# Optimization experiments

Hardware: AMD Instinct MI355X
Metric: run time of the kernel (lower is better)

Reference implementation:

```python
import jax, jax.numpy as jnp
import numpy as np
from functools import partial

N = 50000      # nodes
E = 800000     # edges
B = 64         # graphs in batch
D = 64         # embedding_dim (= per-head out_dim)
H = 2          # num_heads
G = 50         # n_gaussians
HID = 128      # hidden_dim of edge-filter net
MLP_DIM = 128  # mlp_dim of OutputMLP
OUT = 1        # output_dim
L = 3          # n_interactions
CUTOFF = 8.0
MEAN = 0.0
STD = 1.0


def ssp(x):
    # shifted softplus: softplus(x) - log(2)
    return jax.nn.softplus(x) - jnp.log(2.0)


def setup_inputs() -> dict:
    key = jax.random.key(0)
    ks = jax.random.split(key, 24)
    R = jax.random.normal(ks[0], (N, 3), dtype=jnp.float32) * 3.0
    Z = jax.random.randint(ks[1], (N,), 0, 100)
    src = jax.random.randint(ks[2], (E,), 0, N)
    dst = jax.random.randint(ks[3], (E,), 0, N)
    graph_ids = jnp.sort(jax.random.randint(ks[4], (N,), 0, B))
    # embedding table with padding_idx=0 zeroed
    emb_table = (jax.random.normal(ks[5], (100, D), dtype=jnp.float32) * 0.1).at[0].set(0.0)
    offsets = jnp.linspace(0.0, CUTOFF, G, dtype=jnp.float32)
    widths = jnp.full((G,), offsets[1] - offsets[0], dtype=jnp.float32)
    s = 0.1
    rn = lambda k, shp: jax.random.normal(k, shp, dtype=jnp.float32) * s
    return {
        "R": R, "Z": Z, "src": src, "dst": dst, "graph_ids": graph_ids,
        "emb_table": emb_table, "offsets": offsets, "widths": widths,
        "fc_w": rn(ks[6], (L, D, H * D)),
        "attn_l": rn(ks[7], (L, H, D)),
        "attn_r": rn(ks[8], (L, H, D)),
        "filt_w1": rn(ks[9], (L, G, HID)), "filt_b1": jnp.zeros((L, HID), jnp.float32),
        "filt_w2": rn(ks[10], (L, HID, H * D)), "filt_b2": jnp.zeros((L, H * D), jnp.float32),
        "mlp_w1": rn(ks[11], (L, H * D, D)), "mlp_b1": jnp.zeros((L, D), jnp.float32),
        "mlp_w2": rn(ks[12], (L, D, D)), "mlp_b2": jnp.zeros((L, D), jnp.float32),
        "out_w1": rn(ks[13], (D, MLP_DIM)), "out_b1": jnp.zeros((MLP_DIM,), jnp.float32),
        "out_w2": rn(ks[14], (MLP_DIM, OUT)), "out_b2": jnp.zeros((OUT,), jnp.float32),
    }


def _forward(R, emb_table, offsets, widths, fc_w, attn_l, attn_r,
             filt_w1, filt_b1, filt_w2, filt_b2,
             mlp_w1, mlp_b1, mlp_w2, mlp_b2,
             out_w1, out_b1, out_w2, out_b2,
             Z, src, dst, graph_ids):
    # per-edge distances
    r = jnp.linalg.norm(R[src] - R[dst], axis=1)  # (E,)
    # Gaussian smearing (trainable offsets/widths, schnetpack style)
    coeff = -0.5 / (widths ** 2)
    gs = jnp.exp(coeff * (r[:, None] - offsets) ** 2)  # (E, G)
    # cosine cutoff
    C = 0.5 * (jnp.cos(r * (jnp.pi / CUTOFF)) + 1.0) * (r < CUTOFF).astype(r.dtype)  # (E,)
    x = emb_table[Z]  # (N, D)
    for l in range(L):
        h = (x @ fc_w[l]).reshape(N, H, D)  # (N, H, D)
        # cfconv-style edge filter from gaussian features
        w = ssp(gs @ filt_w1[l] + filt_b1[l]) @ filt_w2[l] + filt_b2[l]  # (E, H*D)
        w = w.reshape(E, H, D)
        msg = h[src] * w * C[:, None, None]  # (E, H, D)
        # GAT attention, softmax over incoming edges per dst node
        el = jnp.einsum('nhd,hd->nh', h, attn_l[l])
        er = jnp.einsum('nhd,hd->nh', h, attn_r[l])
        e = jax.nn.leaky_relu(el[src] + er[dst], negative_slope=0.2)  # (E, H)
        m = jax.ops.segment_max(e, dst, num_segments=N)  # (N, H)
        ex = jnp.exp(e - m[dst])
        denom = jax.ops.segment_sum(ex, dst, num_segments=N)  # (N, H)
        alpha = ex / denom[dst]  # (E, H)
        agg = jax.ops.segment_sum(alpha[:, :, None] * msg, dst, num_segments=N)  # (N, H, D)
        v = ssp(agg).reshape(N, H * D)
        v = ssp(v @ mlp_w1[l] + mlp_b1[l]) @ mlp_w2[l] + mlp_b2[l]  # (N, D)
        x = x + v
    hh = ssp(x @ out_w1 + out_b1) @ out_w2 + out_b2  # (N, OUT)
    hh = hh * STD + MEAN
    return jax.ops.segment_sum(hh, graph_ids, num_segments=B)  # (B, OUT)


def reference(R, Z, src, dst, graph_ids, emb_table, offsets, widths,
              fc_w, attn_l, attn_r, filt_w1, filt_b1, filt_w2, filt_b2,
              mlp_w1, mlp_b1, mlp_w2, mlp_b2,
              out_w1, out_b1, out_w2, out_b2):
    return _forward(R, emb_table, offsets, widths, fc_w, attn_l, attn_r,
                    filt_w1, filt_b1, filt_w2, filt_b2,
                    mlp_w1, mlp_b1, mlp_w2, mlp_b2,
                    out_w1, out_b1, out_w2, out_b2,
                    Z, src, dst, graph_ids)
```

## Files before the change

kernel.cpp:

```cpp
#include <hip/hip_runtime.h>
#include <stdint.h>

#define N_NODES 50000
#define N_EDGES 800000
#define B_GRAPHS 64
#define D_DIM 64
#define HD 128
#define G_GAUSS 50
#define HID_DIM 128
#define L_LAYERS 3
#define LN2 0.69314718055994530942f
#define PI_OVER_8 0.39269908169872414f
#define NCHUNK 196

#define TN 64
#define TLD 132
#define XLD 68
#define NBLK ((N_NODES + TN - 1) / TN)

#define LUT_T 2048
#define LUT_INV_STEP 256.0f
#define LROWS 8

__device__ __forceinline__ float sspf(float x) {
    float ax = fabsf(x);
    return fmaxf(x, 0.f) + __logf(1.f + __expf(-ax)) - LN2;
}
__device__ __forceinline__ unsigned short f2bf(float f) {
    union { float f; unsigned int i; } v; v.f = f;
    unsigned int u = v.i;
    return (unsigned short)((u + 0x7FFFu + ((u >> 16) & 1u)) >> 16);
}

__global__ void repr_prep(int* __restrict__ count_f, int* __restrict__ count_s,
                          float* __restrict__ dout) {
    int i = blockIdx.x * 256 + threadIdx.x;
    if (i < N_NODES) count_f[i] = 0;
    else if (i < 2 * N_NODES) count_s[i - N_NODES] = 0;
    else if (i < 2 * N_NODES + B_GRAPHS) dout[i - 2 * N_NODES] = 0.f;
}

__global__ __launch_bounds__(256) void repr_lut_build(
    const float* __restrict__ offs, const float* __restrict__ widths,
    const float* __restrict__ fw1, const float* __restrict__ fb1,
    const float* __restrict__ fw2, const float* __restrict__ fb2,
    unsigned int* __restrict__ lut)
{
    __shared__ float gs_s[LROWS + 1][G_GAUSS];
    __shared__ float hid_s[LROWS + 1][HID_DIM];
    __shared__ float wc_s[LROWS + 1][HD];
    const int nb = LUT_T / LROWS;
    int l = blockIdx.x / nb;
    int i0r = (blockIdx.x % nb) * LROWS;
    int tid = threadIdx.x;
    const float step = 8.0f / LUT_T;

    for (int j = tid; j < (LROWS + 1) * G_GAUSS; j += 256) {
        int r = j / G_GAUSS, k = j - r * G_GAUSS;
        float rr = (i0r + r) * step;
        float wdt = widths[k];
        float dr = rr - offs[k];
        gs_s[r][k] = expf(-0.5f / (wdt * wdt) * dr * dr);
    }
    __syncthreads();

    int c = tid & 127, sub = tid >> 7;
    int rlo = sub * 4;
    {
        const float* W1 = fw1 + (size_t)l * G_GAUSS * HID_DIM + c;
        float acc[5];
        float bb = fb1[l * HID_DIM + c];
        #pragma unroll
        for (int r = 0; r < 5; r++) acc[r] = bb;
        for (int k = 0; k < G_GAUSS; k++) {
            float wv = W1[k * HID_DIM];
            #pragma unroll
            for (int r = 0; r < 5; r++)
                acc[r] = fmaf(gs_s[rlo + r][k], wv, acc[r]);
        }
        #pragma unroll
        for (int r = 0; r < 5; r++) hid_s[rlo + r][c] = sspf(acc[r]);
    }
    __syncthreads();
    {
        const float* W2 = fw2 + (size_t)l * HID_DIM * HD + c;
        float acc[5];
        float bb = fb2[l * HD + c];
        #pragma unroll
        for (int r = 0; r < 5; r++) acc[r] = bb;
        for (int k = 0; k < HID_DIM; k++) {
            float wv = W2[k * HD];
            #pragma unroll
            for (int r = 0; r < 5; r++)
                acc[r] = fmaf(hid_s[rlo + r][k], wv, acc[r]);
        }
        #pragma unroll
        for (int r = 0; r < 5; r++) {
            float rr = (i0r + rlo + r) * step;
            float C = (rr < 8.0f) ? 0.5f * (cosf(rr * PI_OVER_8) + 1.f) : 0.f;
            wc_s[rlo + r][c] = acc[r] * C;
        }
    }
    __syncthreads();
    for (int j = tid; j < LROWS * HD; j += 256) {
        int r = j >> 7, cc = j & 127;
        unsigned int lo = f2bf(wc_s[r][cc]);
        unsigned int hi = f2bf(wc_s[r + 1][cc]);
        lut[((size_t)l * LUT_T + i0r + r) * HD + cc] = lo | (hi << 16);
    }
}

__global__ void repr_hist(const float* __restrict__ R,
                          const int* __restrict__ src, const int* __restrict__ dst,
                          int* __restrict__ count_f, int* __restrict__ count_s,
                          float* __restrict__ r_full) {
    int e = blockIdx.x * blockDim.x + threadIdx.x;
    if (e >= N_EDGES) return;
    int s = src[e], d = dst[e];
    atomicAdd(&count_f[d], 1);
    float dx = R[3*s+0] - R[3*d+0];
    float dy = R[3*s+1] - R[3*d+1];
    float dz = R[3*s+2] - R[3*d+2];
    float r = sqrtf(dx*dx + dy*dy + dz*dz);
    r_full[e] = r;
    if (r < 8.0f) atomicAdd(&count_s[d], 1);
}

__global__ void repr_scanA2(const int* __restrict__ cntA, int* __restrict__ exclA,
                            int* __restrict__ bsumA,
                            const int* __restrict__ cntB, int* __restrict__ exclB,
                            int* __restrict__ bsumB) {
    __shared__ int tmp[256];
    int t = threadIdx.x, b = blockIdx.x;
    const int* cnt; int* excl; int* bsum; int bb;
    if (b < NCHUNK) { cnt = cntA; excl = exclA; bsum = bsumA; bb = b; }
    else            { cnt = cntB; excl = exclB; bsum = bsumB; bb = b - NCHUNK; }
    int i = bb * 256 + t;
    int v = (i < N_NODES) ? cnt[i] : 0;
    tmp[t] = v; __syncthreads();
    for (int off = 1; off < 256; off <<= 1) {
        int add = (t >= off) ? tmp[t - off] : 0;
        __syncthreads();
        tmp[t] += add;
        __syncthreads();
    }
    if (i < N_NODES) excl[i] = tmp[t] - v;
    if (t == 255) bsum[bb] = tmp[255];
}
__global__ void repr_scanB2(const int* __restrict__ bsumA, int* __restrict__ bprefA,
                            int* __restrict__ ecA,
                            const int* __restrict__ bsumB, int* __restrict__ bprefB,
                            int* __restrict__ ecB) {
    __shared__ int tmp[256];
    const int* bsum = blockIdx.x ? bsumB : bsumA;
    int* bpref = blockIdx.x ? bprefB : bprefA;
    int* ec = blockIdx.x ? ecB : ecA;
    int t = threadIdx.x;
    int v = (t < NCHUNK) ? bsum[t] : 0;
    tmp[t] = v; __syncthreads();
    for (int off = 1; off < 256; off <<= 1) {
        int add = (t >= off) ? tmp[t - off] : 0;
        __syncthreads();
        tmp[t] += add;
        __syncthreads();
    }
    if (t < NCHUNK) bpref[t] = tmp[t] - v;
    if (t == 255) ec[0] = tmp[255];
}
__global__ void repr_scanC2(const int* __restrict__ exclA, const int* __restrict__ bprefA,
                            int* __restrict__ curA, int* __restrict__ rowptr,
                            const int* __restrict__ exclB, const int* __restrict__ bprefB,
                            int* __restrict__ curB) {
    int b = blockIdx.x;
    if (b < NCHUNK) {
        int i = b * 256 + threadIdx.x;
        if (i < N_NODES) { int v = exclA[i] + bprefA[b]; curA[i] = v; rowptr[i] = v; }
    } else {
        int i = (b - NCHUNK) * 256 + threadIdx.x;
        if (i < N_NODES) curB[i] = exclB[i] + bprefB[b - NCHUNK];
    }
}

__global__ void repr_scatter(const float* __restrict__ r_full,
                             const int* __restrict__ src, const int* __restrict__ dst,
                             int* __restrict__ cur_f, int* __restrict__ cur_s,
                             unsigned short* __restrict__ ssrc_f,
                             int2* __restrict__ surv) {
    int e = blockIdx.x * blockDim.x + threadIdx.x;
    if (e >= N_EDGES) return;
    int s = src[e], d = dst[e];
    float r = r_full[e];
    int pos = atomicAdd(&cur_f[d], 1);
    ssrc_f[pos] = (unsigned short)s;
    if (r < 8.0f) {
        int p2 = atomicAdd(&cur_s[d], 1);
        unsigned rf = (unsigned)fminf(r * 16777216.f, 134217727.f);
        surv[p2] = make_int2((int)((unsigned)s | ((unsigned)d << 16)), (int)rf);
    }
}


__device__ __forceinline__ void load_ssp_agg(int base, int tid,
        const float* __restrict__ agg, float* __restrict__ bufA) {
    int row = tid >> 2;
    int c0 = (tid & 3) << 5;
    const float* ap = agg + (size_t)(base + row) * HD + c0;
    float* tp = bufA + row * TLD + c0;
    #pragma unroll
    for (int j = 0; j < 8; j++) {
        float4 v = *(const float4*)(ap + j * 4);
        tp[j*4+0] = sspf(v.x); tp[j*4+1] = sspf(v.y);
        tp[j*4+2] = sspf(v.z); tp[j*4+3] = sspf(v.w);
    }
}

__device__ __forceinline__ void gemm_mlp(int base, int tid,
        const float* __restrict__ w1, const float* __restrict__ b1,
        const float* __restrict__ w2, const float* __restrict__ b2,
        float* __restrict__ x, float* __restrict__ bufA, float* __restrict__ v1s)
{
    const int rg = tid >> 4, cg = tid & 15;
    const int r0 = rg * 4, c0 = cg * 4;
    float acc[4][4];
    #pragma unroll
    for (int r = 0; r < 4; r++)
        #pragma unroll
        for (int c = 0; c < 4; c++) acc[r][c] = 0.f;
    for (int k0 = 0; k0 < 128; k0 += 4) {
        float av[4][4];
        #pragma unroll
        for (int r = 0; r < 4; r++)
            *(float4*)av[r] = *(const float4*)&bufA[(r0 + r) * TLD + k0];
        #pragma unroll
        for (int kk = 0; kk < 4; kk++) {
            float4 wv = *(const float4*)(w1 + (k0 + kk) * 64 + c0);
            float wf[4] = {wv.x, wv.y, wv.z, wv.w};
            #pragma unroll
            for (int r = 0; r < 4; r++)
                #pragma unroll
                for (int c = 0; c < 4; c++)
                    acc[r][c] = fmaf(av[r][kk], wf[c], acc[r][c]);
        }
    }
    {
        float4 bv = *(const float4*)(b1 + c0);
        float ba[4] = {bv.x, bv.y, bv.z, bv.w};
        #pragma unroll
        for (int r = 0; r < 4; r++)
            #pragma unroll
            for (int c = 0; c < 4; c++)
                v1s[(r0 + r) * XLD + c0 + c] = sspf(acc[r][c] + ba[c]);
    }
    __syncthreads();
    float acc2[4][4];
    #pragma unroll
    for (int r = 0; r < 4; r++)
        #pragma unroll
        for (int c = 0; c < 4; c++) acc2[r][c] = 0.f;
    for (int k0 = 0; k0 < 64; k0 += 4) {
        float av[4][4];
        #pragma unroll
        for (int r = 0; r < 4; r++)
            *(float4*)av[r] = *(const float4*)&v1s[(r0 + r) * XLD + k0];
        #pragma unroll
        for (int kk = 0; kk < 4; kk++) {
            float4 wv = *(const float4*)(w2 + (k0 + kk) * 64 + c0);
            float wf[4] = {wv.x, wv.y, wv.z, wv.w};
            #pragma unroll
            for (int r = 0; r < 4; r++)
                #pragma unroll
                for (int c = 0; c < 4; c++)
                    acc2[r][c] = fmaf(av[r][kk], wf[c], acc2[r][c]);
        }
    }
    {
        float4 bv = *(const float4*)(b2 + c0);
        #pragma unroll
        for (int r = 0; r < 4; r++) {
            int n = base + r0 + r;
            float4 xv = *(const float4*)(x + (size_t)n * 64 + c0);
            float4 o;
            o.x = acc2[r][0] + bv.x + xv.x;
            o.y = acc2[r][1] + bv.y + xv.y;
            o.z = acc2[r][2] + bv.z + xv.z;
            o.w = acc2[r][3] + bv.w + xv.w;
            *(float4*)&bufA[(r0 + r) * XLD + c0] = o;
            if (n < N_NODES) *(float4*)(x + (size_t)n * 64 + c0) = o;
        }
    }
    __syncthreads();
}

__device__ __forceinline__ void gemm_h(int base, int tid,
        const float* __restrict__ bufA,
        const float* __restrict__ fc_w, const float* __restrict__ attn_l,
        const float* __restrict__ attn_r,
        unsigned int* __restrict__ hq, float* __restrict__ el, float* __restrict__ er)
{
    const int rg = tid >> 4, cg = tid & 15;
    const int r0 = rg * 4, c0 = cg * 8;
    float acc[4][8];
    #pragma unroll
    for (int r = 0; r < 4; r++)
        #pragma unroll
        for (int c = 0; c < 8; c++) acc[r][c] = 0.f;
    for (int k0 = 0; k0 < 64; k0 += 4) {
        float av[4][4];
        #pragma unroll
        for (int r = 0; r < 4; r++)
            *(float4*)av[r] = *(const float4*)&bufA[(r0 + r) * XLD + k0];
        #pragma unroll
        for (int kk = 0; kk < 4; kk++) {
            float4 w0 = *(const float4*)(fc_w + (k0 + kk) * 128 + c0);
            float4 w1v = *(const float4*)(fc_w + (k0 + kk) * 128 + c0 + 4);
            float wf[8] = {w0.x, w0.y, w0.z, w0.w, w1v.x, w1v.y, w1v.z, w1v.w};
            #pragma unroll
            for (int r = 0; r < 4; r++)
                #pragma unroll
                for (int c = 0; c < 8; c++)
                    acc[r][c] = fmaf(av[r][kk], wf[c], acc[r][c]);
        }
    }
    float al[8], ar[8];
    #pragma unroll
    for (int c = 0; c < 8; c++) { al[c] = attn_l[c0 + c]; ar[c] = attn_r[c0 + c]; }
    int head = cg >> 3;
    #pragma unroll
    for (int r = 0; r < 4; r++) {
        int n = base + r0 + r;
        float pel = 0.f, per = 0.f;
        #pragma unroll
        for (int c = 0; c < 8; c++) {
            pel = fmaf(acc[r][c], al[c], pel);
            per = fmaf(acc[r][c], ar[c], per);
        }
        if (n < N_NODES) {
            uint4 pv;
            pv.x = (unsigned int)f2bf(acc[r][0]) | ((unsigned int)f2bf(acc[r][1]) << 16);
            pv.y = (unsigned int)f2bf(acc[r][2]) | ((unsigned int)f2bf(acc[r][3]) << 16);
            pv.z = (unsigned int)f2bf(acc[r][4]) | ((unsigned int)f2bf(acc[r][5]) << 16);
            pv.w = (unsigned int)f2bf(acc[r][6]) | ((unsigned int)f2bf(acc[r][7]) << 16);
            *(uint4*)(hq + (size_t)n * 64 + cg * 4) = pv;
        }
        #pragma unroll
        for (int off = 1; off < 8; off <<= 1) {
            pel += __shfl_xor(pel, off, 64);
            per += __shfl_xor(per, off, 64);
        }
        if ((cg & 7) == 0 && n < N_NODES) {
            el[n * 2 + head] = pel;
            er[n * 2 + head] = per;
        }
    }
}

__global__ __launch_bounds__(256) void repr_embed_h(
        const float* __restrict__ emb, const int* __restrict__ Z,
        const float* __restrict__ fc_w, const float* __restrict__ attn_l,
        const float* __restrict__ attn_r,
        float* __restrict__ x, unsigned int* __restrict__ hq,
        float* __restrict__ el, float* __restrict__ er) {
    __shared__ float bufA[TN * XLD];
    int base = blockIdx.x * TN, tid = threadIdx.x;
    int row = tid >> 2;
    int c0 = (tid & 3) << 4;
    int n = base + row;
    int z = (n < N_NODES) ? Z[n] : 0;
    const float* ep = emb + (size_t)z * D_DIM + c0;
    float* bp = bufA + row * XLD + c0;
    #pragma unroll
    for (int j = 0; j < 4; j++) {
        float4 v = *(const float4*)(ep + j * 4);
        *(float4*)(bp + j * 4) = v;
        if (n < N_NODES) *(float4*)(x + (size_t)n * D_DIM + c0 + j * 4) = v;
    }
    __syncthreads();
    gemm_h(base, tid, bufA, fc_w, attn_l, attn_r, hq, el, er);
}

__global__ __launch_bounds__(256) void repr_mlp_h(
        const float* __restrict__ agg,
        const float* __restrict__ w1, const float* __restrict__ b1,
        const float* __restrict__ w2, const float* __restrict__ b2,
        const float* __restrict__ fc_w, const float* __restrict__ attn_l,
        const float* __restrict__ attn_r,
        float* __restrict__ x, unsigned int* __restrict__ hq,
        float* __restrict__ el, float* __restrict__ er) {
    __shared__ float bufA[TN * TLD];
    __shared__ float v1s[TN * XLD];
    int base = blockIdx.x * TN, tid = threadIdx.x;
    load_ssp_agg(base, tid, agg, bufA);
    __syncthreads();
    gemm_mlp(base, tid, w1, b1, w2, b2, x, bufA, v1s);
    gemm_h(base, tid, bufA, fc_w, attn_l, attn_r, hq, el, er);
}

__global__ __launch_bounds__(256) void repr_mlp_out(
        const float* __restrict__ agg,
        const float* __restrict__ w1, const float* __restrict__ b1,
        const float* __restrict__ w2, const float* __restrict__ b2,
        const float* __restrict__ ow1, const float* __restrict__ ob1,
        const float* __restrict__ ow2, const float* __restrict__ ob2,
        float* __restrict__ x, float* __restrict__ hh) {
    __shared__ float bufA[TN * TLD];
    __shared__ float v1s[TN * XLD];
    int base = blockIdx.x * TN, tid = threadIdx.x;
    load_ssp_agg(base, tid, agg, bufA);
    __syncthreads();
    gemm_mlp(base, tid, w1, b1, w2, b2, x, bufA, v1s);
    const int rg = tid >> 4, cg = tid & 15;
    const int r0 = rg * 4, c0 = cg * 8;
    float acc[4][8];
    #pragma unroll
    for (int r = 0; r < 4; r++)
        #pragma unroll
        for (int c = 0; c < 8; c++) acc[r][c] = 0.f;
    for (int k0 = 0; k0 < 64; k0 += 4) {
        float av[4][4];
        #pragma unroll
        for (int r = 0; r < 4; r++)
            *(float4*)av[r] = *(const float4*)&bufA[(r0 + r) * XLD + k0];
        #pragma unroll
        for (int kk = 0; kk < 4; kk++) {
            float4 w0 = *(const float4*)(ow1 + (k0 + kk) * 128 + c0);
            float4 w1v = *(const float4*)(ow1 + (k0 + kk) * 128 + c0 + 4);
            float wf[8] = {w0.x, w0.y, w0.z, w0.w, w1v.x, w1v.y, w1v.z, w1v.w};
            #pragma unroll
            for (int r = 0; r < 4; r++)
                #pragma unroll
                for (int c = 0; c < 8; c++)
                    acc[r][c] = fmaf(av[r][kk], wf[c], acc[r][c]);
        }
    }
    float o1[8], w2c[8];
    #pragma unroll
    for (int c = 0; c < 8; c++) { o1[c] = ob1[c0 + c]; w2c[c] = ow2[c0 + c]; }
    #pragma unroll
    for (int r = 0; r < 4; r++) {
        int n = base + r0 + r;
        float s = 0.f;
        #pragma unroll
        for (int c = 0; c < 8; c++)
            s = fmaf(sspf(acc[r][c] + o1[c]), w2c[c], s);
        #pragma unroll
        for (int off = 1; off < 16; off <<= 1)
            s += __shfl_xor(s, off, 64);
        if (cg == 0 && n < N_NODES) hh[n] = s + ob2[0];
    }
}

__global__ void repr_alpha(const unsigned short* __restrict__ ssrc_f,
                           const int* __restrict__ rowptr,
                           const float* __restrict__ el, const float* __restrict__ er,
                           float2* __restrict__ md, float* __restrict__ agg) {
    int t = blockIdx.x * 256 + threadIdx.x;
    int d = t >> 4;
    int lane16 = t & 15;
    if (d >= N_NODES) return;
    float4 z = make_float4(0.f, 0.f, 0.f, 0.f);
    float4* ar = (float4*)(agg + (size_t)d * HD);
    ar[lane16 * 2] = z;
    ar[lane16 * 2 + 1] = z;
    int rs = rowptr[d];
    int re = (d == N_NODES - 1) ? N_EDGES : rowptr[d + 1];
    float2 erd = *(const float2*)&er[2 * d];
    float s0 = 0.f, s1 = 0.f;
    for (int i = rs + lane16; i < re; i += 16) {
        int s = ssrc_f[i];
        float2 a = *(const float2*)&el[2 * s];
        float v0 = a.x + erd.x; v0 = v0 >= 0.f ? v0 : 0.2f * v0;
        float v1 = a.y + erd.y; v1 = v1 >= 0.f ? v1 : 0.2f * v1;
        s0 += __expf(v0);
        s1 += __expf(v1);
    }
    #pragma unroll
    for (int off = 8; off > 0; off >>= 1) {
        s0 += __shfl_xor(s0, off, 64);
        s1 += __shfl_xor(s1, off, 64);
    }
    if (lane16 == 0) md[d] = make_float2(1.f / s0, 1.f / s1);
}

#define TILE 64
__global__ __launch_bounds__(256) void repr_msg_lut(
    const int2* __restrict__ surv, const int* __restrict__ ecount,
    const float* __restrict__ el, const float* __restrict__ er,
    const float2* __restrict__ md, const unsigned int* __restrict__ hq,
    const unsigned int* __restrict__ lut,
    float* __restrict__ agg)
{
    __shared__ int4 rowinfo[TILE];
    __shared__ float scl[TILE][2];
    int EC = ecount[0];
    int base = blockIdx.x * TILE;
    if (base >= EC) return;
    int tid = threadIdx.x;
    if (tid < TILE) {
        int i = base + tid;
        int sn = 0, d = -1, i0 = 0;
        float fr = 0.f, sc0 = 0.f, sc1 = 0.f;
        if (i < EC) {
            int2 ev = surv[i];
            sn = (int)((unsigned)ev.x & 0xFFFFu);
            d  = (int)((unsigned)ev.x >> 16);
            unsigned rf = (unsigned)ev.y;
            i0 = (int)(rf >> 16);
            fr = (float)(rf & 0xFFFFu) * (1.f / 65536.f);
            float2 a = *(const float2*)&el[2 * sn];
            float2 b = *(const float2*)&er[2 * d];
            float2 rd = md[d];
            float v0 = a.x + b.x; v0 = v0 >= 0.f ? v0 : 0.2f * v0;
            float v1 = a.y + b.y; v1 = v1 >= 0.f ? v1 : 0.2f * v1;
            sc0 = __expf(v0) * rd.x;
            sc1 = __expf(v1) * rd.y;
        }
        rowinfo[tid] = make_int4(i0, sn, d, __float_as_int(fr));
        scl[tid][0] = sc0; scl[tid][1] = sc1;
    }
    __syncthreads();
    const int cp = tid & 63;
    const int sp = tid >> 6;
    const int head = cp >> 5;
    const int lo = sp * 16;
    const uint2* __restrict__ l2p = (const uint2*)lut;
    float sum0 = 0.f, sum1 = 0.f;
    int cur_d = -1;
    int seg_first = 1;
    #pragma unroll 4
    for (int j = 0; j < 16; j++) {
        int r = lo + j;
        int4 ri = rowinfo[r];
        if (ri.z != cur_d) {
            if (cur_d >= 0) {
                float* ap = &agg[(size_t)cur_d * HD + 2 * cp];
                if (seg_first) { atomicAdd(ap, sum0); atomicAdd(ap + 1, sum1); }
                else *(float2*)ap = make_float2(sum0, sum1);
            }
            cur_d = ri.z; sum0 = 0.f; sum1 = 0.f; seg_first = (j == 0);
        }
        if (ri.z >= 0) {
            uint2 tv = l2p[(size_t)ri.x * 64 + cp];
            float fr = __int_as_float(ri.w);
            float wa0 = __uint_as_float(tv.x << 16);
            float wa1 = __uint_as_float(tv.x & 0xFFFF0000u);
            float wb0 = __uint_as_float(tv.y << 16);
            float wb1 = __uint_as_float(tv.y & 0xFFFF0000u);
            unsigned int hv = hq[(size_t)ri.y * 64 + cp];
            float ha = __uint_as_float(hv << 16);
            float hb = __uint_as_float(hv & 0xFFFF0000u);
            float s = scl[r][head];
            float wa = fmaf(fr, wa1 - wa0, wa0);
            float wb = fmaf(fr, wb1 - wb0, wb0);
            sum0 = fmaf(wa * ha, s, sum0);
            sum1 = fmaf(wb * hb, s, sum1);
        }
    }
    if (cur_d >= 0) {
        float* ap = &agg[(size_t)cur_d * HD + 2 * cp];
        atomicAdd(ap, sum0); atomicAdd(ap + 1, sum1);
    }
}

__global__ void repr_gsum(const float* __restrict__ hh, const int* __restrict__ gids,
                          float* __restrict__ dout) {
    __shared__ float bins[B_GRAPHS];
    int t = threadIdx.x;
    if (t < B_GRAPHS) bins[t] = 0.f;
    __syncthreads();
    int i = blockIdx.x * 256 + t;
    if (i < N_NODES) atomicAdd(&bins[gids[i]], hh[i]);
    __syncthreads();
    if (t < B_GRAPHS && bins[t] != 0.f) atomicAdd(&dout[t], bins[t]);
}

extern "C" void kernel_launch(void* const* d_in, const int* in_sizes, int n_in,
                              void* d_out, int out_size, void* d_ws, size_t ws_size,
                              hipStream_t stream) {
    (void)in_sizes; (void)n_in; (void)out_size; (void)ws_size;
    const float* R      = (const float*)d_in[0];
    const int*   Z      = (const int*)d_in[1];
    const int*   src    = (const int*)d_in[2];
    const int*   dst    = (const int*)d_in[3];
    const int*   gids   = (const int*)d_in[4];
    const float* emb    = (const float*)d_in[5];
    const float* offs   = (const float*)d_in[6];
    const float* widths = (const float*)d_in[7];
    const float* fc_w   = (const float*)d_in[8];
    const float* attn_l = (const float*)d_in[9];
    const float* attn_r = (const float*)d_in[10];
    const float* fw1    = (const float*)d_in[11];
    const float* fb1    = (const float*)d_in[12];
    const float* fw2    = (const float*)d_in[13];
    const float* fb2    = (const float*)d_in[14];
    const float* mw1    = (const float*)d_in[15];
    const float* mb1    = (const float*)d_in[16];
    const float* mw2    = (const float*)d_in[17];
    const float* mb2    = (const float*)d_in[18];
    const float* ow1    = (const float*)d_in[19];
    const float* ob1    = (const float*)d_in[20];
    const float* ow2    = (const float*)d_in[21];
    const float* ob2    = (const float*)d_in[22];

    char* p = (char*)d_ws;
    float* x      = (float*)p; p += (size_t)N_NODES * 64 * 4;
    unsigned int* hq = (unsigned int*)p; p += (size_t)N_NODES * 64 * 4;
    float* el     = (float*)p; p += (size_t)N_NODES * 2 * 4;
    float* er     = (float*)p; p += (size_t)N_NODES * 2 * 4;
    float2* md    = (float2*)p; p += (size_t)N_NODES * 8;
    float* agg    = (float*)p; p += (size_t)N_NODES * 128 * 4;
    unsigned short* ssrc_f = (unsigned short*)p; p += (size_t)N_EDGES * 2;
    int*   rowptr = (int*)p;   p += (size_t)N_NODES * 4;
    int2*  surv   = (int2*)p;  p += (size_t)N_EDGES * 8;
    float* r_full = (float*)p; p += (size_t)N_EDGES * 4;
    float* hh     = (float*)p; p += (size_t)N_NODES * 4;
    int*   bsumA  = (int*)p;   p += 1024;
    int*   bprefA = (int*)p;   p += 1024;
    int*   bsumB  = (int*)p;   p += 1024;
    int*   bprefB = (int*)p;   p += 1024;
    int*   ecF    = (int*)p;   p += 256;
    int*   ecS    = (int*)p;   p += 256;
    unsigned int* lut = (unsigned int*)r_full;
    int* count_f = (int*)x;
    int* excl_f  = (int*)((char*)x + 256 * 1024);
    int* cur_f   = (int*)((char*)x + 512 * 1024);
    int* count_s = (int*)((char*)x + 768 * 1024);
    int* excl_s  = (int*)((char*)x + 1024 * 1024);
    int* cur_s   = (int*)((char*)x + 1280 * 1024);

    repr_prep<<<(2 * N_NODES + B_GRAPHS + 255) / 256, 256, 0, stream>>>(
        count_f, count_s, (float*)d_out);
    repr_hist<<<N_EDGES / 256, 256, 0, stream>>>(R, src, dst, count_f, count_s, r_full);
    repr_scanA2<<<2 * NCHUNK, 256, 0, stream>>>(count_f, excl_f, bsumA,
                                                count_s, excl_s, bsumB);
    repr_scanB2<<<2, 256, 0, stream>>>(bsumA, bprefA, ecF, bsumB, bprefB, ecS);
    repr_scanC2<<<2 * NCHUNK, 256, 0, stream>>>(excl_f, bprefA, cur_f, rowptr,
                                                excl_s, bprefB, cur_s);
    repr_scatter<<<N_EDGES / 256, 256, 0, stream>>>(
        r_full, src, dst, cur_f, cur_s, ssrc_f, surv);

    repr_lut_build<<<L_LAYERS * (LUT_T / LROWS), 256, 0, stream>>>(
        offs, widths, fw1, fb1, fw2, fb2, lut);

    repr_embed_h<<<NBLK, 256, 0, stream>>>(
        emb, Z, fc_w, attn_l, attn_r, x, hq, el, er);

    for (int l = 0; l < L_LAYERS; l++) {
        repr_alpha<<<(N_NODES * 16 + 255) / 256, 256, 0, stream>>>(
            ssrc_f, rowptr, el, er, md, agg);
        repr_msg_lut<<<N_EDGES / TILE, 256, 0, stream>>>(
            surv, ecS, el, er, md, hq,
            lut + (size_t)l * LUT_T * HD, agg);
        if (l < L_LAYERS - 1) {
            repr_mlp_h<<<NBLK, 256, 0, stream>>>(
                agg, mw1 + (size_t)l * 128 * 64, mb1 + l * 64,
                mw2 + (size_t)l * 64 * 64, mb2 + l * 64,
                fc_w + (size_t)(l + 1) * 64 * 128, attn_l + (l + 1) * 128,
                attn_r + (l + 1) * 128, x, hq, el, er);
        } else {
            repr_mlp_out<<<NBLK, 256, 0, stream>>>(
                agg, mw1 + (size_t)l * 128 * 64, mb1 + l * 64,
                mw2 + (size_t)l * 64 * 64, mb2 + l * 64,
                ow1, ob1, ow2, ob2, x, hh);
        }
    }
    repr_gsum<<<NCHUNK, 256, 0, stream>>>(hh, gids, (float*)d_out);
}
```

Measured before the change: 692.0 us.

## Replace full-graph CSR softmax denominator with per-edge atomic accumulation

Drops the full-edge CSR build (count, scan and scatter for all edges) and its dst-sorted source array. Each layer now computes the softmax denominator with a per-edge kernel that atomically adds exp values into a per-node buffer. A second small kernel inverts the sums, resets the buffer and zeroes agg. This removes the setup cost of the second CSR pass but adds float atomics on 800k edges per layer, with random el gathers. The summation order also becomes nondeterministic.

```diff
diff --git a/kernel.cpp b/kernel.cpp
--- a/kernel.cpp
+++ b/kernel.cpp
@@ -19,7 +19,6 @@
 #define NBLK ((N_NODES + TN - 1) / TN)
 
 #define LUT_T 2048
-#define LUT_INV_STEP 256.0f
 #define LROWS 8
 
 __device__ __forceinline__ float sspf(float x) {
@@ -32,12 +31,12 @@
     return (unsigned short)((u + 0x7FFFu + ((u >> 16) & 1u)) >> 16);
 }
 
-__global__ void repr_prep(int* __restrict__ count_f, int* __restrict__ count_s,
+__global__ void repr_prep(int* __restrict__ count_s, float* __restrict__ denom,
                           float* __restrict__ dout) {
     int i = blockIdx.x * 256 + threadIdx.x;
-    if (i < N_NODES) count_f[i] = 0;
-    else if (i < 2 * N_NODES) count_s[i - N_NODES] = 0;
-    else if (i < 2 * N_NODES + B_GRAPHS) dout[i - 2 * N_NODES] = 0.f;
+    if (i < N_NODES) count_s[i] = 0;
+    else if (i < 3 * N_NODES) denom[i - N_NODES] = 0.f;
+    else if (i < 3 * N_NODES + B_GRAPHS) dout[i - 3 * N_NODES] = 0.f;
 }
 
 __global__ __launch_bounds__(256) void repr_lut_build(
@@ -112,12 +111,11 @@
 
 __global__ void repr_hist(const float* __restrict__ R,
                           const int* __restrict__ src, const int* __restrict__ dst,
-                          int* __restrict__ count_f, int* __restrict__ count_s,
+                          int* __restrict__ count_s,
                           float* __restrict__ r_full) {
     int e = blockIdx.x * blockDim.x + threadIdx.x;
     if (e >= N_EDGES) return;
     int s = src[e], d = dst[e];
-    atomicAdd(&count_f[d], 1);
     float dx = R[3*s+0] - R[3*d+0];
     float dy = R[3*s+1] - R[3*d+1];
     float dz = R[3*s+2] - R[3*d+2];
@@ -126,16 +124,11 @@
     if (r < 8.0f) atomicAdd(&count_s[d], 1);
 }
 
-__global__ void repr_scanA2(const int* __restrict__ cntA, int* __restrict__ exclA,
-                            int* __restrict__ bsumA,
-                            const int* __restrict__ cntB, int* __restrict__ exclB,
-                            int* __restrict__ bsumB) {
+__global__ void repr_scanA(const int* __restrict__ cnt, int* __restrict__ excl,
+                           int* __restrict__ bsum) {
     __shared__ int tmp[256];
     int t = threadIdx.x, b = blockIdx.x;
-    const int* cnt; int* excl; int* bsum; int bb;
-    if (b < NCHUNK) { cnt = cntA; excl = exclA; bsum = bsumA; bb = b; }
-    else            { cnt = cntB; excl = exclB; bsum = bsumB; bb = b - NCHUNK; }
-    int i = bb * 256 + t;
+    int i = b * 256 + t;
     int v = (i < N_NODES) ? cnt[i] : 0;
     tmp[t] = v; __syncthreads();
     for (int off = 1; off < 256; off <<= 1) {
@@ -145,16 +138,11 @@
         __syncthreads();
     }
     if (i < N_NODES) excl[i] = tmp[t] - v;
-    if (t == 255) bsum[bb] = tmp[255];
-}
-__global__ void repr_scanB2(const int* __restrict__ bsumA, int* __restrict__ bprefA,
-                            int* __restrict__ ecA,
-                            const int* __restrict__ bsumB, int* __restrict__ bprefB,
-                            int* __restrict__ ecB) {
+    if (t == 255) bsum[b] = tmp[255];
+}
+__global__ void repr_scanB(const int* __restrict__ bsum, int* __restrict__ bpref,
+                           int* __restrict__ ec) {
     __shared__ int tmp[256];
-    const int* bsum = blockIdx.x ? bsumB : bsumA;
-    int* bpref = blockIdx.x ? bprefB : bprefA;
-    int* ec = blockIdx.x ? ecB : ecA;
     int t = threadIdx.x;
     int v = (t < NCHUNK) ? bsum[t] : 0;
     tmp[t] = v; __syncthreads();
@@ -167,32 +155,21 @@
     if (t < NCHUNK) bpref[t] = tmp[t] - v;
     if (t == 255) ec[0] = tmp[255];
 }
-__global__ void repr_scanC2(const int* __restrict__ exclA, const int* __restrict__ bprefA,
-                            int* __restrict__ curA, int* __restrict__ rowptr,
-                            const int* __restrict__ exclB, const int* __restrict__ bprefB,
-                            int* __restrict__ curB) {
-    int b = blockIdx.x;
-    if (b < NCHUNK) {
-        int i = b * 256 + threadIdx.x;
-        if (i < N_NODES) { int v = exclA[i] + bprefA[b]; curA[i] = v; rowptr[i] = v; }
-    } else {
-        int i = (b - NCHUNK) * 256 + threadIdx.x;
-        if (i < N_NODES) curB[i] = exclB[i] + bprefB[b - NCHUNK];
-    }
+__global__ void repr_scanC(const int* __restrict__ excl, const int* __restrict__ bpref,
+                           int* __restrict__ cur) {
+    int i = blockIdx.x * 256 + threadIdx.x;
+    if (i < N_NODES) cur[i] = excl[i] + bpref[blockIdx.x];
 }
 
 __global__ void repr_scatter(const float* __restrict__ r_full,
                              const int* __restrict__ src, const int* __restrict__ dst,
-                             int* __restrict__ cur_f, int* __restrict__ cur_s,
-                             unsigned short* __restrict__ ssrc_f,
+                             int* __restrict__ cur_s,
                              int2* __restrict__ surv) {
     int e = blockIdx.x * blockDim.x + threadIdx.x;
     if (e >= N_EDGES) return;
-    int s = src[e], d = dst[e];
     float r = r_full[e];
-    int pos = atomicAdd(&cur_f[d], 1);
-    ssrc_f[pos] = (unsigned short)s;
     if (r < 8.0f) {
+        int s = src[e], d = dst[e];
         int p2 = atomicAdd(&cur_s[d], 1);
         unsigned rf = (unsigned)fminf(r * 16777216.f, 134217727.f);
         surv[p2] = make_int2((int)((unsigned)s | ((unsigned)d << 16)), (int)rf);
@@ -449,10 +426,22 @@
     }
 }
 
-__global__ void repr_alpha(const unsigned short* __restrict__ ssrc_f,
-                           const int* __restrict__ rowptr,
-                           const float* __restrict__ el, const float* __restrict__ er,
-                           float2* __restrict__ md, float* __restrict__ agg) {
+__global__ void repr_alpha_e(const int* __restrict__ src, const int* __restrict__ dst,
+                             const float* __restrict__ el, const float* __restrict__ er,
+                             float* __restrict__ denom) {
+    int e = blockIdx.x * 256 + threadIdx.x;
+    if (e >= N_EDGES) return;
+    int s = src[e], d = dst[e];
+    float2 a = *(const float2*)&el[2 * s];
+    float2 b = *(const float2*)&er[2 * d];
+    float v0 = a.x + b.x; v0 = v0 >= 0.f ? v0 : 0.2f * v0;
+    float v1 = a.y + b.y; v1 = v1 >= 0.f ? v1 : 0.2f * v1;
+    atomicAdd(&denom[2 * d],     __expf(v0));
+    atomicAdd(&denom[2 * d + 1], __expf(v1));
+}
+
+__global__ void repr_mdk(float* __restrict__ denom, float2* __restrict__ md,
+                         float* __restrict__ agg) {
     int t = blockIdx.x * 256 + threadIdx.x;
     int d = t >> 4;
     int lane16 = t & 15;
@@ -461,24 +450,11 @@
     float4* ar = (float4*)(agg + (size_t)d * HD);
     ar[lane16 * 2] = z;
     ar[lane16 * 2 + 1] = z;
-    int rs = rowptr[d];
-    int re = (d == N_NODES - 1) ? N_EDGES : rowptr[d + 1];
-    float2 erd = *(const float2*)&er[2 * d];
-    float s0 = 0.f, s1 = 0.f;
-    for (int i = rs + lane16; i < re; i += 16) {
-        int s = ssrc_f[i];
-        float2 a = *(const float2*)&el[2 * s];
-        float v0 = a.x + erd.x; v0 = v0 >= 0.f ? v0 : 0.2f * v0;
-        float v1 = a.y + erd.y; v1 = v1 >= 0.f ? v1 : 0.2f * v1;
-        s0 += __expf(v0);
-        s1 += __expf(v1);
-    }
-    #pragma unroll
-    for (int off = 8; off > 0; off >>= 1) {
-        s0 += __shfl_xor(s0, off, 64);
-        s1 += __shfl_xor(s1, off, 64);
-    }
-    if (lane16 == 0) md[d] = make_float2(1.f / s0, 1.f / s1);
+    if (lane16 == 0) {
+        float2 dn = *(const float2*)&denom[2 * d];
+        md[d] = make_float2(1.f / dn.x, 1.f / dn.y);
+        *(float2*)&denom[2 * d] = make_float2(0.f, 0.f);
+    }
 }
 
 #define TILE 64
@@ -607,36 +583,27 @@
     float* el     = (float*)p; p += (size_t)N_NODES * 2 * 4;
     float* er     = (float*)p; p += (size_t)N_NODES * 2 * 4;
     float2* md    = (float2*)p; p += (size_t)N_NODES * 8;
+    float* denom  = (float*)p; p += (size_t)N_NODES * 2 * 4;
     float* agg    = (float*)p; p += (size_t)N_NODES * 128 * 4;
-    unsigned short* ssrc_f = (unsigned short*)p; p += (size_t)N_EDGES * 2;
-    int*   rowptr = (int*)p;   p += (size_t)N_NODES * 4;
     int2*  surv   = (int2*)p;  p += (size_t)N_EDGES * 8;
     float* r_full = (float*)p; p += (size_t)N_EDGES * 4;
     float* hh     = (float*)p; p += (size_t)N_NODES * 4;
-    int*   bsumA  = (int*)p;   p += 1024;
-    int*   bprefA = (int*)p;   p += 1024;
-    int*   bsumB  = (int*)p;   p += 1024;
-    int*   bprefB = (int*)p;   p += 1024;
-    int*   ecF    = (int*)p;   p += 256;
+    int*   bsum   = (int*)p;   p += 1024;
+    int*   bpref  = (int*)p;   p += 1024;
     int*   ecS    = (int*)p;   p += 256;
     unsigned int* lut = (unsigned int*)r_full;
-    int* count_f = (int*)x;
-    int* excl_f  = (int*)((char*)x + 256 * 1024);
-    int* cur_f   = (int*)((char*)x + 512 * 1024);
-    int* count_s = (int*)((char*)x + 768 * 1024);
-    int* excl_s  = (int*)((char*)x + 1024 * 1024);
-    int* cur_s   = (int*)((char*)x + 1280 * 1024);
-
-    repr_prep<<<(2 * N_NODES + B_GRAPHS + 255) / 256, 256, 0, stream>>>(
-        count_f, count_s, (float*)d_out);
-    repr_hist<<<N_EDGES / 256, 256, 0, stream>>>(R, src, dst, count_f, count_s, r_full);
-    repr_scanA2<<<2 * NCHUNK, 256, 0, stream>>>(count_f, excl_f, bsumA,
-                                                count_s, excl_s, bsumB);
-    repr_scanB2<<<2, 256, 0, stream>>>(bsumA, bprefA, ecF, bsumB, bprefB, ecS);
-    repr_scanC2<<<2 * NCHUNK, 256, 0, stream>>>(excl_f, bprefA, cur_f, rowptr,
-                                                excl_s, bprefB, cur_s);
+    int* count_s = (int*)x;
+    int* excl_s  = (int*)((char*)x + 256 * 1024);
+    int* cur_s   = (int*)((char*)x + 512 * 1024);
+
+    repr_prep<<<(3 * N_NODES + B_GRAPHS + 255) / 256, 256, 0, stream>>>(
+        count_s, denom, (float*)d_out);
+    repr_hist<<<N_EDGES / 256, 256, 0, stream>>>(R, src, dst, count_s, r_full);
+    repr_scanA<<<NCHUNK, 256, 0, stream>>>(count_s, excl_s, bsum);
+    repr_scanB<<<1, 256, 0, stream>>>(bsum, bpref, ecS);
+    repr_scanC<<<NCHUNK, 256, 0, stream>>>(excl_s, bpref, cur_s);
     repr_scatter<<<N_EDGES / 256, 256, 0, stream>>>(
-        r_full, src, dst, cur_f, cur_s, ssrc_f, surv);
+        r_full, src, dst, cur_s, surv);
 
     repr_lut_build<<<L_LAYERS * (LUT_T / LROWS), 256, 0, stream>>>(
         offs, widths, fw1, fb1, fw2, fb2, lut);
@@ -645,8 +612,10 @@
         emb, Z, fc_w, attn_l, attn_r, x, hq, el, er);
 
     for (int l = 0; l < L_LAYERS; l++) {
-        repr_alpha<<<(N_NODES * 16 + 255) / 256, 256, 0, stream>>>(
-            ssrc_f, rowptr, el, er, md, agg);
+        repr_alpha_e<<<(N_EDGES + 255) / 256, 256, 0, stream>>>(
+            src, dst, el, er, denom);
+        repr_mdk<<<(N_NODES * 16 + 255) / 256, 256, 0, stream>>>(
+            denom, md, agg);
         repr_msg_lut<<<N_EDGES / TILE, 256, 0, stream>>>(
             surv, ecS, el, er, md, hq,
             lut + (size_t)l * LUT_T * HD, agg);
```

Result: slower. 855.6 us (+23.6%).
